# Performance work log

Measured on AMD Instinct MI355X. Metric: run time of the kernel, lower is better.

The kernel has to match this reference:

```python
import jax, jax.numpy as jnp
import numpy as np

QUERY_DIM = 256
CONTEXT_DIM = 256
N_HEADS = 4
D_HEAD = QUERY_DIM // N_HEADS
LN_EPS = 1e-5


def setup_inputs() -> dict:
    key = jax.random.key(0)
    ks = jax.random.split(key, 8)
    B, L, Nv = 4, 8192, 8
    query = jax.random.normal(ks[0], (B, L, QUERY_DIM), dtype=jnp.float32)
    context = jax.random.normal(ks[1], (B, L, Nv, CONTEXT_DIM), dtype=jnp.float32)
    s = 1.0 / np.sqrt(CONTEXT_DIM)
    Wk = jax.random.uniform(ks[2], (CONTEXT_DIM, QUERY_DIM), jnp.float32, -s, s)
    bk = jax.random.uniform(ks[3], (QUERY_DIM,), jnp.float32, -s, s)
    Wv = jax.random.uniform(ks[4], (CONTEXT_DIM, QUERY_DIM), jnp.float32, -s, s)
    bv = jax.random.uniform(ks[5], (QUERY_DIM,), jnp.float32, -s, s)
    gamma = jnp.ones((QUERY_DIM,), jnp.float32)
    beta = jnp.zeros((QUERY_DIM,), jnp.float32)
    return {"query": query, "context": context, "Wk": Wk, "bk": bk,
            "Wv": Wv, "bv": bv, "gamma": gamma, "beta": beta}


def reference(query, context, Wk, bk, Wv, bv, gamma, beta):
    B, L, C = query.shape
    Nv = context.shape[2]
    # LayerNorm over channel dim
    mu = jnp.mean(query, axis=-1, keepdims=True)
    var = jnp.mean(jnp.square(query - mu), axis=-1, keepdims=True)
    q = (query - mu) * jax.lax.rsqrt(var + LN_EPS) * gamma + beta
    # projections: [B,L,Nv,C]
    k = context @ Wk + bk
    v = context @ Wv + bv
    q = q.reshape(B, L, N_HEADS, D_HEAD)
    k = k.reshape(B, L, Nv, N_HEADS, D_HEAD)
    v = v.reshape(B, L, Nv, N_HEADS, D_HEAD)
    # per-token attention over the Nv local context elements
    scores = jnp.einsum('blhd,blnhd->bhln', q, k) / np.sqrt(D_HEAD)
    probs = jax.nn.softmax(scores, axis=-1)  # [B,H,L,Nv]
    out = jnp.einsum('bhln,blnhd->blhd', probs, v).reshape(B, L, C)
    return out, probs
```

## Files before the change

kernel.cpp:

```cpp
#include <hip/hip_runtime.h>
#include <math.h>

#define TB     16
#define CDIM   256
#define NHEADS 4
#define DHEAD  64
#define NV     8
#define LSEQ   8192
#define NB     4

typedef short  bf16x8 __attribute__((ext_vector_type(8)));
typedef float  f32x4  __attribute__((ext_vector_type(4)));
typedef unsigned short u16;

static __device__ __forceinline__ u16 f2bf(float x) {
    unsigned u = __float_as_uint(x);
    unsigned r = ((u >> 16) & 1u) + 0x7fffu;
    return (u16)((u + r) >> 16);
}

__global__ __launch_bounds__(256) void prep_frags(
    const float* __restrict__ Wk, const float* __restrict__ Wv,
    u16* __restrict__ wkf, u16* __restrict__ wvf)
{
    const int tid = blockIdx.x * 256 + threadIdx.x;
    union { u16 u[8]; uint4 v; } pk;
    if (tid < 8192) {
        const int l = tid & 63;
        int r = tid >> 6;
        const int nt = r & 15; r >>= 4;
        const int kc = r & 1;  r >>= 1;
        const int h  = r & 3;
        const int c     = nt * 16 + (l & 15);
        const int dbase = h * DHEAD + kc * 32 + (l >> 4) * 8;
        #pragma unroll
        for (int j = 0; j < 8; ++j)
            pk.u[j] = f2bf(Wk[(size_t)c * CDIM + dbase + j] * 0.125f);
        const size_t unit = (size_t)(tid >> 6) * 128 + l;
        *reinterpret_cast<uint4*>(wkf + unit * 8) = pk.v;
    } else {
        const int t2 = tid - 8192;
        const int l = t2 & 63;
        int r = t2 >> 6;
        const int nt = r & 3; r >>= 2;
        const int kc = r & 7; r >>= 3;
        const int h  = r & 3;
        const int d     = h * DHEAD + nt * 16 + (l & 15);
        const int cbase = kc * 32 + (l >> 4) * 8;
        #pragma unroll
        for (int j = 0; j < 8; ++j)
            pk.u[j] = f2bf(Wv[(size_t)(cbase + j) * CDIM + d]);
        const size_t unit = (size_t)(t2 >> 6) * 128 + l;
        *reinterpret_cast<uint4*>(wvf + unit * 8) = pk.v;
    }
}

__global__ __launch_bounds__(1024, 8) void triplane_fused(
    const float* __restrict__ q,
    const float* __restrict__ ctx,
    const u16*   __restrict__ wkf,
    const u16*   __restrict__ wvf,
    const float* __restrict__ bv,
    const float* __restrict__ gamma,
    const float* __restrict__ beta,
    float* __restrict__ out,
    float* __restrict__ probs_out)
{
    __shared__ __align__(16) float s_qk[TB * NHEADS * CDIM];
    __shared__ __align__(16) u16   s_qnh[TB * CDIM];

    const int tid  = threadIdx.x;
    const int w    = tid >> 6;
    const int lane = tid & 63;
    const int tok0 = blockIdx.x * TB;
    const f32x4 zero4 = {0.f, 0.f, 0.f, 0.f};

    const int h  = w & 3;
    const int cq = w >> 2;

    {
        const int t = w;
        const int c = lane * 4;
        const float4 qv = *reinterpret_cast<const float4*>(q + (size_t)(tok0 + t) * CDIM + c);
        float s  = qv.x + qv.y + qv.z + qv.w;
        float s2 = qv.x*qv.x + qv.y*qv.y + qv.z*qv.z + qv.w*qv.w;
        #pragma unroll
        for (int off = 32; off >= 1; off >>= 1) {
            s  += __shfl_xor(s,  off);
            s2 += __shfl_xor(s2, off);
        }
        const float mu   = s  * (1.0f / CDIM);
        const float var  = s2 * (1.0f / CDIM) - mu * mu;
        const float rstd = rsqrtf(var + 1e-5f);
        const float4 g  = *reinterpret_cast<const float4*>(gamma + c);
        const float4 be = *reinterpret_cast<const float4*>(beta + c);
        ushort4 vh;
        vh.x = f2bf((qv.x - mu) * rstd * g.x + be.x);
        vh.y = f2bf((qv.y - mu) * rstd * g.y + be.y);
        vh.z = f2bf((qv.z - mu) * rstd * g.z + be.z);
        vh.w = f2bf((qv.w - mu) * rstd * g.w + be.w);
        const int off = t * 512 + ((lane * 8) ^ (t << 4));
        *reinterpret_cast<ushort4*>(reinterpret_cast<char*>(s_qnh) + off) = vh;
    }
    __syncthreads();

    {
        const int arow = lane & 15;
        const int akq  = lane >> 4;
        bf16x8 aH[2];
        #pragma unroll
        for (int kc = 0; kc < 2; ++kc) {
            const int intra = (h * DHEAD + kc * 32 + akq * 8) * 2;
            const int off   = arow * 512 + (intra ^ (arow << 4));
            aH[kc] = *reinterpret_cast<const bf16x8*>(reinterpret_cast<const char*>(s_qnh) + off);
        }
        __builtin_amdgcn_s_setprio(1);
        #pragma unroll
        for (int nt = 0; nt < 4; ++nt) {
            const int ntg = cq * 4 + nt;
            f32x4 acc = zero4;
            #pragma unroll
            for (int kc = 0; kc < 2; ++kc) {
                const u16* p = wkf + ((size_t)(h * 4096 + kc * 2048 + ntg * 128) + lane) * 8;
                const bf16x8 bH = *reinterpret_cast<const bf16x8*>(p);
                acc = __builtin_amdgcn_mfma_f32_16x16x32_bf16(aH[kc], bH, acc, 0, 0, 0);
            }
            const int cc = ntg * 16 + (lane & 15);
            #pragma unroll
            for (int reg = 0; reg < 4; ++reg) {
                const int t = (lane >> 4) * 4 + reg;
                s_qk[(t * NHEADS + h) * CDIM + cc] = acc[reg];
            }
        }
        __builtin_amdgcn_s_setprio(0);
    }
    __syncthreads();

    float p0, p1, p2, p3;
    {
        const int t  = w;
        const int cs = lane & 7;
        const float* cb = ctx + ((size_t)(tok0 + t) * NV + (lane >> 3)) * CDIM + cs * 4;
        p0 = 0.f; p1 = 0.f; p2 = 0.f; p3 = 0.f;
        #pragma unroll
        for (int i = 0; i < 8; ++i) {
            const int c = i * 32 + cs * 4;
            const float4 cv = *reinterpret_cast<const float4*>(cb + i * 32);
            const float4 k0 = *reinterpret_cast<const float4*>(&s_qk[(t*NHEADS+0)*CDIM + c]);
            const float4 k1 = *reinterpret_cast<const float4*>(&s_qk[(t*NHEADS+1)*CDIM + c]);
            const float4 k2 = *reinterpret_cast<const float4*>(&s_qk[(t*NHEADS+2)*CDIM + c]);
            const float4 k3 = *reinterpret_cast<const float4*>(&s_qk[(t*NHEADS+3)*CDIM + c]);
            p0 += cv.x*k0.x + cv.y*k0.y + cv.z*k0.z + cv.w*k0.w;
            p1 += cv.x*k1.x + cv.y*k1.y + cv.z*k1.z + cv.w*k1.w;
            p2 += cv.x*k2.x + cv.y*k2.y + cv.z*k2.z + cv.w*k2.w;
            p3 += cv.x*k3.x + cv.y*k3.y + cv.z*k3.z + cv.w*k3.w;
        }
        #pragma unroll
        for (int off = 4; off >= 1; off >>= 1) {
            p0 += __shfl_xor(p0, off);
            p1 += __shfl_xor(p1, off);
            p2 += __shfl_xor(p2, off);
            p3 += __shfl_xor(p3, off);
        }
        float m0 = p0, m1 = p1, m2 = p2, m3 = p3;
        #pragma unroll
        for (int off = 8; off <= 32; off <<= 1) {
            m0 = fmaxf(m0, __shfl_xor(m0, off));
            m1 = fmaxf(m1, __shfl_xor(m1, off));
            m2 = fmaxf(m2, __shfl_xor(m2, off));
            m3 = fmaxf(m3, __shfl_xor(m3, off));
        }
        p0 = __expf(p0 - m0); p1 = __expf(p1 - m1);
        p2 = __expf(p2 - m2); p3 = __expf(p3 - m3);
        float s0 = p0, s1 = p1, s2 = p2, s3 = p3;
        #pragma unroll
        for (int off = 8; off <= 32; off <<= 1) {
            s0 += __shfl_xor(s0, off);
            s1 += __shfl_xor(s1, off);
            s2 += __shfl_xor(s2, off);
            s3 += __shfl_xor(s3, off);
        }
        p0 /= s0; p1 /= s1; p2 /= s2; p3 /= s3;
    }

    {
        const int t = w;
        const float* cbase = ctx + ((size_t)(tok0 + t) * NV) * CDIM + lane * 4;
        float4 a0, a1, a2, a3;
        a0.x=a0.y=a0.z=a0.w=0.f; a1=a0; a2=a0; a3=a0;
        #pragma unroll
        for (int n = 0; n < NV; ++n) {
            const float prx = __shfl(p0, n * 8);
            const float pry = __shfl(p1, n * 8);
            const float prz = __shfl(p2, n * 8);
            const float prw = __shfl(p3, n * 8);
            const float4 cv = *reinterpret_cast<const float4*>(cbase + (size_t)n * CDIM);
            a0.x += prx*cv.x; a0.y += prx*cv.y; a0.z += prx*cv.z; a0.w += prx*cv.w;
            a1.x += pry*cv.x; a1.y += pry*cv.y; a1.z += pry*cv.z; a1.w += pry*cv.w;
            a2.x += prz*cv.x; a2.y += prz*cv.y; a2.z += prz*cv.z; a2.w += prz*cv.w;
            a3.x += prw*cv.x; a3.y += prw*cv.y; a3.z += prw*cv.z; a3.w += prw*cv.w;
        }
        char* base = reinterpret_cast<char*>(s_qk) + t * 4096;
        const int xo = (lane * 8) ^ ((t & 7) << 4);
        #pragma unroll
        for (int hh = 0; hh < 4; ++hh) {
            const float4 v = (hh == 0) ? a0 : (hh == 1) ? a1 : (hh == 2) ? a2 : a3;
            ushort4 vh;
            vh.x = f2bf(v.x); vh.y = f2bf(v.y); vh.z = f2bf(v.z); vh.w = f2bf(v.w);
            *reinterpret_cast<ushort4*>(base + hh * 512 + xo) = vh;
        }
    }
    __syncthreads();

    {
        const int arow = lane & 15;
        const int akq  = lane >> 4;
        const int nt   = cq;
        const char* wch = reinterpret_cast<const char*>(s_qk);
        const u16* wvbase = wvf + ((size_t)(h * 4096) + lane) * 8;
        f32x4 acc = zero4;
        __builtin_amdgcn_s_setprio(1);
        #pragma unroll
        for (int kc = 0; kc < 8; ++kc) {
            const int intra = kc * 64 + akq * 16;
            const int off   = arow * 4096 + h * 512 + (intra ^ ((arow & 7) << 4));
            const bf16x8 aH = *reinterpret_cast<const bf16x8*>(wch + off);
            const u16* pp = wvbase + (size_t)(kc * 512 + nt * 128) * 8;
            const bf16x8 bH = *reinterpret_cast<const bf16x8*>(pp);
            acc = __builtin_amdgcn_mfma_f32_16x16x32_bf16(aH, bH, acc, 0, 0, 0);
        }
        __builtin_amdgcn_s_setprio(0);
        const int d = h * DHEAD + nt * 16 + (lane & 15);
        const float bvv = bv[d];
        #pragma unroll
        for (int reg = 0; reg < 4; ++reg) {
            const int t = (lane >> 4) * 4 + reg;
            out[(size_t)(tok0 + t) * CDIM + d] = acc[reg] + bvv;
        }
    }

    {
        const int cs = lane & 7;
        if (cs == 0) {
            const int t = w;
            const int tok = tok0 + t;
            const int b = tok >> 13;
            const int l = tok & (LSEQ - 1);
            const int n = lane >> 3;
            float* pb = probs_out + (((size_t)b * NHEADS) * LSEQ + l) * NV + n;
            pb[0 * LSEQ * NV] = p0;
            pb[1 * LSEQ * NV] = p1;
            pb[2 * LSEQ * NV] = p2;
            pb[3 * LSEQ * NV] = p3;
        }
    }
}

static __device__ __forceinline__ float bf2f_fb(u16 h) {
    return __uint_as_float(((unsigned)h) << 16);
}
#define TBF 8
__global__ __launch_bounds__(512, 6) void triplane_fused_v1(
    const float* __restrict__ q, const float* __restrict__ ctx,
    const float* __restrict__ Wk, const float* __restrict__ Wv,
    const float* __restrict__ bv, const float* __restrict__ gamma,
    const float* __restrict__ beta, float* __restrict__ out,
    float* __restrict__ probs_out)
{
    __shared__ float s_qn[TBF * CDIM];
    __shared__ float s_qk[TBF * NHEADS * CDIM];
    __shared__ float s_sc[TBF * NV * NHEADS];
    const int tid  = threadIdx.x;
    const int w    = tid >> 6;
    const int lane = tid & 63;
    const int tok0 = blockIdx.x * TBF;
    {
        const int t = w; const int c = lane * 4;
        const float4 qv = *reinterpret_cast<const float4*>(q + (size_t)(tok0 + t) * CDIM + c);
        float s  = qv.x + qv.y + qv.z + qv.w;
        float s2 = qv.x*qv.x + qv.y*qv.y + qv.z*qv.z + qv.w*qv.w;
        #pragma unroll
        for (int off = 32; off >= 1; off >>= 1) { s += __shfl_xor(s, off); s2 += __shfl_xor(s2, off); }
        const float mu = s * (1.0f/CDIM);
        const float var = s2 * (1.0f/CDIM) - mu*mu;
        const float rstd = rsqrtf(var + 1e-5f);
        const float4 g  = *reinterpret_cast<const float4*>(gamma + c);
        const float4 be = *reinterpret_cast<const float4*>(beta + c);
        float4 qn;
        qn.x=(qv.x-mu)*rstd*g.x+be.x; qn.y=(qv.y-mu)*rstd*g.y+be.y;
        qn.z=(qv.z-mu)*rstd*g.z+be.z; qn.w=(qv.w-mu)*rstd*g.w+be.w;
        *reinterpret_cast<float4*>(&s_qn[t*CDIM + c]) = qn;
    }
    __syncthreads();
    {
        const int h = w & 3; const int cg = w >> 2;
        const int c0 = cg*128 + lane; const int c1 = c0 + 64;
        const float* wk0 = Wk + (size_t)c0*CDIM + h*DHEAD;
        const float* wk1 = Wk + (size_t)c1*CDIM + h*DHEAD;
        float acc0[TBF], acc1[TBF];
        #pragma unroll
        for (int t = 0; t < TBF; ++t) { acc0[t]=0.f; acc1[t]=0.f; }
        for (int d4 = 0; d4 < DHEAD/4; ++d4) {
            const float4 wa = *reinterpret_cast<const float4*>(wk0 + d4*4);
            const float4 wb = *reinterpret_cast<const float4*>(wk1 + d4*4);
            #pragma unroll
            for (int t = 0; t < TBF; ++t) {
                const float4 qv = *reinterpret_cast<const float4*>(&s_qn[t*CDIM + h*DHEAD + d4*4]);
                acc0[t] += qv.x*wa.x + qv.y*wa.y + qv.z*wa.z + qv.w*wa.w;
                acc1[t] += qv.x*wb.x + qv.y*wb.y + qv.z*wb.z + qv.w*wb.w;
            }
        }
        #pragma unroll
        for (int t = 0; t < TBF; ++t) {
            s_qk[(t*NHEADS+h)*CDIM + c0] = acc0[t];
            s_qk[(t*NHEADS+h)*CDIM + c1] = acc1[t];
        }
    }
    __syncthreads();
    {
        const int t = w; const int n = lane >> 3; const int cs = lane & 7;
        const float* cb = ctx + ((size_t)(tok0 + t)*NV + n)*CDIM;
        float p0=0,p1=0,p2=0,p3=0;
        #pragma unroll
        for (int i = 0; i < 8; ++i) {
            const int c = i*32 + cs*4;
            const float4 cv = *reinterpret_cast<const float4*>(cb + c);
            const float4 k0 = *reinterpret_cast<const float4*>(&s_qk[(t*NHEADS+0)*CDIM + c]);
            const float4 k1 = *reinterpret_cast<const float4*>(&s_qk[(t*NHEADS+1)*CDIM + c]);
            const float4 k2 = *reinterpret_cast<const float4*>(&s_qk[(t*NHEADS+2)*CDIM + c]);
            const float4 k3 = *reinterpret_cast<const float4*>(&s_qk[(t*NHEADS+3)*CDIM + c]);
            p0 += cv.x*k0.x+cv.y*k0.y+cv.z*k0.z+cv.w*k0.w;
            p1 += cv.x*k1.x+cv.y*k1.y+cv.z*k1.z+cv.w*k1.w;
            p2 += cv.x*k2.x+cv.y*k2.y+cv.z*k2.z+cv.w*k2.w;
            p3 += cv.x*k3.x+cv.y*k3.y+cv.z*k3.z+cv.w*k3.w;
        }
        #pragma unroll
        for (int off = 4; off >= 1; off >>= 1) {
            p0 += __shfl_xor(p0, off); p1 += __shfl_xor(p1, off);
            p2 += __shfl_xor(p2, off); p3 += __shfl_xor(p3, off);
        }
        if (cs == 0) {
            s_sc[(t*NV+n)*NHEADS+0] = p0*0.125f; s_sc[(t*NV+n)*NHEADS+1] = p1*0.125f;
            s_sc[(t*NV+n)*NHEADS+2] = p2*0.125f; s_sc[(t*NV+n)*NHEADS+3] = p3*0.125f;
        }
    }
    __syncthreads();
    float* s_out = s_qn;
    {
        float4 z; z.x=z.y=z.z=z.w=0.f;
        reinterpret_cast<float4*>(s_out)[tid] = z;
        if (tid < TBF*NHEADS) {
            const int t = tid >> 2; const int h = tid & 3;
            float sc[NV]; float m = -1e30f;
            #pragma unroll
            for (int n = 0; n < NV; ++n) { sc[n] = s_sc[(t*NV+n)*NHEADS+h]; m = fmaxf(m, sc[n]); }
            float sum = 0.f;
            #pragma unroll
            for (int n = 0; n < NV; ++n) { sc[n] = __expf(sc[n]-m); sum += sc[n]; }
            const float inv = 1.f/sum;
            const int tok = tok0 + t; const int b = tok >> 13; const int l = tok & (LSEQ-1);
            float* pdst = probs_out + (((size_t)b*NHEADS + h)*LSEQ + l)*NV;
            #pragma unroll
            for (int n = 0; n < NV; ++n) { const float p = sc[n]*inv; s_sc[(t*NV+n)*NHEADS+h] = p; pdst[n] = p; }
        }
    }
    __syncthreads();
    {
        const int t = w;
        const float* cbase = ctx + ((size_t)(tok0 + t)*NV)*CDIM;
        float4 a0,a1,a2,a3; a0.x=a0.y=a0.z=a0.w=0.f; a1=a0; a2=a0; a3=a0;
        for (int n = 0; n < NV; ++n) {
            const float4 pr = *reinterpret_cast<const float4*>(&s_sc[(t*NV+n)*NHEADS]);
            const float4 cv = *reinterpret_cast<const float4*>(cbase + (size_t)n*CDIM + lane*4);
            a0.x+=pr.x*cv.x; a0.y+=pr.x*cv.y; a0.z+=pr.x*cv.z; a0.w+=pr.x*cv.w;
            a1.x+=pr.y*cv.x; a1.y+=pr.y*cv.y; a1.z+=pr.y*cv.z; a1.w+=pr.y*cv.w;
            a2.x+=pr.z*cv.x; a2.y+=pr.z*cv.y; a2.z+=pr.z*cv.z; a2.w+=pr.z*cv.w;
            a3.x+=pr.w*cv.x; a3.y+=pr.w*cv.y; a3.z+=pr.w*cv.z; a3.w+=pr.w*cv.w;
        }
        *reinterpret_cast<float4*>(&s_qk[(t*NHEADS+0)*CDIM + lane*4]) = a0;
        *reinterpret_cast<float4*>(&s_qk[(t*NHEADS+1)*CDIM + lane*4]) = a1;
        *reinterpret_cast<float4*>(&s_qk[(t*NHEADS+2)*CDIM + lane*4]) = a2;
        *reinterpret_cast<float4*>(&s_qk[(t*NHEADS+3)*CDIM + lane*4]) = a3;
    }
    __syncthreads();
    {
        const int h = w & 3; const int cg = w >> 2;
        float acc[TBF];
        #pragma unroll
        for (int t = 0; t < TBF; ++t) acc[t] = 0.f;
        const float* wvbase = Wv + h*DHEAD + lane;
        for (int c4 = 0; c4 < 32; ++c4) {
            const int c = cg*128 + c4*4;
            const float wv0 = wvbase[(size_t)(c+0)*CDIM];
            const float wv1 = wvbase[(size_t)(c+1)*CDIM];
            const float wv2 = wvbase[(size_t)(c+2)*CDIM];
            const float wv3 = wvbase[(size_t)(c+3)*CDIM];
            #pragma unroll
            for (int t = 0; t < TBF; ++t) {
                const float4 wc = *reinterpret_cast<const float4*>(&s_qk[(t*NHEADS+h)*CDIM + c]);
                acc[t] += wc.x*wv0 + wc.y*wv1 + wc.z*wv2 + wc.w*wv3;
            }
        }
        #pragma unroll
        for (int t = 0; t < TBF; ++t) atomicAdd(&s_out[t*CDIM + h*DHEAD + lane], acc[t]);
    }
    __syncthreads();
    {
        const int t = w; const int c = lane * 4;
        float4 o = *reinterpret_cast<const float4*>(&s_out[t*CDIM + c]);
        const float4 bvv = *reinterpret_cast<const float4*>(bv + c);
        o.x += bvv.x; o.y += bvv.y; o.z += bvv.z; o.w += bvv.w;
        *reinterpret_cast<float4*>(out + (size_t)(tok0 + t)*CDIM + c) = o;
    }
}

extern "C" void kernel_launch(void* const* d_in, const int* in_sizes, int n_in,
                              void* d_out, int out_size, void* d_ws, size_t ws_size,
                              hipStream_t stream) {
    const float* q     = (const float*)d_in[0];
    const float* ctx   = (const float*)d_in[1];
    const float* Wk    = (const float*)d_in[2];
    const float* Wv    = (const float*)d_in[4];
    const float* bv    = (const float*)d_in[5];
    const float* gamma = (const float*)d_in[6];
    const float* beta  = (const float*)d_in[7];

    float* out   = (float*)d_out;
    float* probs = out + (size_t)NB * LSEQ * CDIM;

    const int n_tok = NB * LSEQ;
    const size_t ws_need = (size_t)2 * 131072 * sizeof(u16);

    if (d_ws != nullptr && ws_size >= ws_need) {
        u16* wkf = (u16*)d_ws;
        u16* wvf = wkf + 131072;
        hipLaunchKernelGGL(prep_frags, dim3(64), dim3(256), 0, stream, Wk, Wv, wkf, wvf);
        hipLaunchKernelGGL(triplane_fused, dim3(n_tok / TB), dim3(1024), 0, stream,
                           q, ctx, wkf, wvf, bv, gamma, beta, out, probs);
    } else {
        hipLaunchKernelGGL(triplane_fused_v1, dim3(n_tok / TBF), dim3(512), 0, stream,
                           q, ctx, Wk, Wv, bv, gamma, beta, out, probs);
    }
}
```

Measured before the change: 96.89 us.

## Prefetch first context chunk to LDS asynchronously and store qk as bf16

Issues async global-to-LDS loads for the first 64 channels of each token's context rows before the qK MFMA stage, so part of the context fetch overlaps that compute. The qk projection buffer in shared memory is stored as bf16 instead of fp32, halving its LDS footprint, which makes room for the staging buffer. The scores loop reads the first two chunks from LDS and the rest from global. Storing qk in bf16 lowers score precision, and there is no explicit wait on the async load before it is read beyond the existing barrier.

Result: no change. 96.45 us (-0.5%).

```diff
diff --git a/kernel.cpp b/kernel.cpp
--- a/kernel.cpp
+++ b/kernel.cpp
@@ -18,6 +18,18 @@
     unsigned r = ((u >> 16) & 1u) + 0x7fffu;
     return (u16)((u + r) >> 16);
 }
+static __device__ __forceinline__ float bf2f(u16 h) {
+    return __uint_as_float(((unsigned)h) << 16);
+}
+static __device__ __forceinline__ float4 ld_bf4(const u16* p) {
+    const ushort4 v = *reinterpret_cast<const ushort4*>(p);
+    float4 r;
+    r.x = bf2f(v.x); r.y = bf2f(v.y); r.z = bf2f(v.z); r.w = bf2f(v.w);
+    return r;
+}
+
+typedef __attribute__((address_space(1))) const void glds_src_t;
+typedef __attribute__((address_space(3))) void glds_dst_t;
 
 __global__ __launch_bounds__(256) void prep_frags(
     const float* __restrict__ Wk, const float* __restrict__ Wv,
@@ -66,8 +78,9 @@
     float* __restrict__ out,
     float* __restrict__ probs_out)
 {
-    __shared__ __align__(16) float s_qk[TB * NHEADS * CDIM];
+    __shared__ __align__(16) u16   s_qkh[TB * NHEADS * CDIM];
     __shared__ __align__(16) u16   s_qnh[TB * CDIM];
+    __shared__ __align__(16) float s_ctx[TB * NV * 64];
 
     const int tid  = threadIdx.x;
     const int w    = tid >> 6;
@@ -105,6 +118,16 @@
     __syncthreads();
 
     {
+        const int t = w;
+        const float* gsrc = ctx + ((size_t)(tok0 + t) * NV + (lane >> 4)) * CDIM + (lane & 15) * 4;
+        char* ldst = reinterpret_cast<char*>(s_ctx) + t * 2048;
+        __builtin_amdgcn_global_load_lds((glds_src_t*)gsrc,
+                                         (glds_dst_t*)ldst, 16, 0, 0);
+        __builtin_amdgcn_global_load_lds((glds_src_t*)(gsrc + 4 * CDIM),
+                                         (glds_dst_t*)(ldst + 1024), 16, 0, 0);
+    }
+
+    {
         const int arow = lane & 15;
         const int akq  = lane >> 4;
         bf16x8 aH[2];
@@ -129,7 +152,7 @@
             #pragma unroll
             for (int reg = 0; reg < 4; ++reg) {
                 const int t = (lane >> 4) * 4 + reg;
-                s_qk[(t * NHEADS + h) * CDIM + cc] = acc[reg];
+                s_qkh[(t * NHEADS + h) * CDIM + cc] = f2bf(acc[reg]);
             }
         }
         __builtin_amdgcn_s_setprio(0);
@@ -139,17 +162,22 @@
     float p0, p1, p2, p3;
     {
         const int t  = w;
+        const int n  = lane >> 3;
         const int cs = lane & 7;
-        const float* cb = ctx + ((size_t)(tok0 + t) * NV + (lane >> 3)) * CDIM + cs * 4;
+        const float* cb = ctx + ((size_t)(tok0 + t) * NV + n) * CDIM + cs * 4;
+        const float* sc = s_ctx + t * 512 + n * 64 + cs * 4;
+        const u16* kb = s_qkh + (size_t)t * NHEADS * CDIM;
         p0 = 0.f; p1 = 0.f; p2 = 0.f; p3 = 0.f;
         #pragma unroll
         for (int i = 0; i < 8; ++i) {
             const int c = i * 32 + cs * 4;
-            const float4 cv = *reinterpret_cast<const float4*>(cb + i * 32);
-            const float4 k0 = *reinterpret_cast<const float4*>(&s_qk[(t*NHEADS+0)*CDIM + c]);
-            const float4 k1 = *reinterpret_cast<const float4*>(&s_qk[(t*NHEADS+1)*CDIM + c]);
-            const float4 k2 = *reinterpret_cast<const float4*>(&s_qk[(t*NHEADS+2)*CDIM + c]);
-            const float4 k3 = *reinterpret_cast<const float4*>(&s_qk[(t*NHEADS+3)*CDIM + c]);
+            const float4 cv = (i < 2)
+                ? *reinterpret_cast<const float4*>(sc + i * 32)
+                : *reinterpret_cast<const float4*>(cb + i * 32);
+            const float4 k0 = ld_bf4(kb + 0 * CDIM + c);
+            const float4 k1 = ld_bf4(kb + 1 * CDIM + c);
+            const float4 k2 = ld_bf4(kb + 2 * CDIM + c);
+            const float4 k3 = ld_bf4(kb + 3 * CDIM + c);
             p0 += cv.x*k0.x + cv.y*k0.y + cv.z*k0.z + cv.w*k0.w;
             p1 += cv.x*k1.x + cv.y*k1.y + cv.z*k1.z + cv.w*k1.w;
             p2 += cv.x*k2.x + cv.y*k2.y + cv.z*k2.z + cv.w*k2.w;
@@ -200,7 +228,7 @@
             a2.x += prz*cv.x; a2.y += prz*cv.y; a2.z += prz*cv.z; a2.w += prz*cv.w;
             a3.x += prw*cv.x; a3.y += prw*cv.y; a3.z += prw*cv.z; a3.w += prw*cv.w;
         }
-        char* base = reinterpret_cast<char*>(s_qk) + t * 4096;
+        char* base = reinterpret_cast<char*>(s_qkh) + t * 2048;
         const int xo = (lane * 8) ^ ((t & 7) << 4);
         #pragma unroll
         for (int hh = 0; hh < 4; ++hh) {
@@ -216,14 +244,14 @@
         const int arow = lane & 15;
         const int akq  = lane >> 4;
         const int nt   = cq;
-        const char* wch = reinterpret_cast<const char*>(s_qk);
+        const char* wch = reinterpret_cast<const char*>(s_qkh);
         const u16* wvbase = wvf + ((size_t)(h * 4096) + lane) * 8;
         f32x4 acc = zero4;
         __builtin_amdgcn_s_setprio(1);
         #pragma unroll
         for (int kc = 0; kc < 8; ++kc) {
             const int intra = kc * 64 + akq * 16;
-            const int off   = arow * 4096 + h * 512 + (intra ^ ((arow & 7) << 4));
+            const int off   = arow * 2048 + h * 512 + (intra ^ ((arow & 7) << 4));
             const bf16x8 aH = *reinterpret_cast<const bf16x8*>(wch + off);
             const u16* pp = wvbase + (size_t)(kc * 512 + nt * 128) * 8;
             const bf16x8 bH = *reinterpret_cast<const bf16x8*>(pp);
@@ -256,9 +284,6 @@
     }
 }
 
-static __device__ __forceinline__ float bf2f_fb(u16 h) {
-    return __uint_as_float(((unsigned)h) << 16);
-}
 #define TBF 8
 __global__ __launch_bounds__(512, 6) void triplane_fused_v1(
     const float* __restrict__ q, const float* __restrict__ ctx,
```
